# Kernel tuning notes

Hardware: AMD Instinct MI355X
Metric: run time of the kernel (lower is better)

Reference implementation:

```python
import jax, jax.numpy as jnp
import numpy as np

NEG_BIG = -9e15
ALPHA = 0.2  # LeakyReLU slope


def setup_inputs() -> dict:
    key = jax.random.key(0)
    k1, k2, k3, k4 = jax.random.split(key, 4)
    B, N, Fin, Fout = 8, 2048, 256, 64
    h = jax.random.normal(k1, (B, N, Fin), dtype=jnp.float32)
    adj = jax.random.randint(k2, (B, N, N), 0, 2, dtype=jnp.int32)
    # xavier_uniform-ish scale for W and a
    W = jax.random.normal(k3, (Fin, Fout), dtype=jnp.float32) * (1.414 * np.sqrt(2.0 / (Fin + Fout)))
    a = jax.random.normal(k4, (2 * Fout, 1), dtype=jnp.float32) * (1.414 * np.sqrt(2.0 / (2 * Fout + 1)))
    return {"h": h, "adj": adj, "W": W, "a": a}


def reference(h, adj, W, a):
    Fout = W.shape[1]
    Wh = jnp.einsum("bnf,fo->bno", h, W)  # [B,N,Fout]
    # Decompose concat-based score: a_input @ a == Wh@a1 (src) + Wh@a2 (dst)
    a1, a2 = a[:Fout, 0], a[Fout:, 0]
    e_src = Wh @ a1  # [B,N]
    e_dst = Wh @ a2  # [B,N]
    e = e_src[:, :, None] + e_dst[:, None, :]  # [B,N,N]
    e = jnp.where(e > 0, e, ALPHA * e)  # LeakyReLU
    scores = jnp.where(adj > 0, e, NEG_BIG)
    attention = jax.nn.softmax(scores, axis=-1)  # [B,N,N]
    h_prime = jnp.einsum("bnm,bmo->bno", attention, Wh)
    return jax.nn.elu(h_prime)  # concat=True
```

## Files before the change

kernel.cpp:

```cpp
#include <hip/hip_runtime.h>

#define L2E 1.44269504088896340736f

typedef float f32x4 __attribute__((ext_vector_type(4)));
typedef __bf16 bf16x8 __attribute__((ext_vector_type(8)));
typedef __bf16 bf16x4 __attribute__((ext_vector_type(4)));

__device__ inline void mfma_bf16(bf16x8 a, bf16x8 b, f32x4& c) {
    c = __builtin_amdgcn_mfma_f32_16x16x32_bf16(a, b, c, 0, 0, 0);
}


__global__ __launch_bounds__(256, 2)
void k1_wh(const float* __restrict__ h, const float* __restrict__ W,
           const float* __restrict__ a, __bf16* __restrict__ whP,
           float* __restrict__ esrc, float* __restrict__ edst) {
    const int tid  = threadIdx.x;
    const int lane = tid & 63;
    const int w    = tid >> 6;
    const int blk  = blockIdx.x;
    const int r0   = blk * 8;
    const int b    = r0 >> 11;
    const int n0   = r0 & 2047;

    __shared__ float pt_s[8][4][64];
    __shared__ float whs[64][8];

    float wreg[64];
    {
        const float* Wp = W + (size_t)(w * 64) * 64 + lane;
#pragma unroll
        for (int kk = 0; kk < 64; kk++) wreg[kk] = Wp[(size_t)kk * 64];
    }

    const float* hbase = h + (size_t)r0 * 256 + w * 64;
    for (int rr = 0; rr < 8; rr++) {
        const float4* hp = (const float4*)(hbase + rr * 256);
        float acc = 0.f;
#pragma unroll
        for (int q = 0; q < 16; q++) {
            float4 hv = hp[q];
            acc += hv.x * wreg[4 * q + 0];
            acc += hv.y * wreg[4 * q + 1];
            acc += hv.z * wreg[4 * q + 2];
            acc += hv.w * wreg[4 * q + 3];
        }
        pt_s[rr][w][lane] = acc;
    }
    __syncthreads();

    const float a1 = a[lane];
    const float a2 = a[64 + lane];
#pragma unroll
    for (int rq = 0; rq < 2; rq++) {
        const int rr = w * 2 + rq;
        float v = pt_s[rr][0][lane] + pt_s[rr][1][lane] +
                  pt_s[rr][2][lane] + pt_s[rr][3][lane];
        whs[lane][rr] = v;
        float e1 = v * a1, e2 = v * a2;
#pragma unroll
        for (int d = 1; d < 64; d <<= 1) {
            e1 += __shfl_xor(e1, d);
            e2 += __shfl_xor(e2, d);
        }
        if (lane == 0) { esrc[r0 + rr] = e1; edst[r0 + rr] = e2; }
    }
    __syncthreads();

    if (tid < 128) {
        const int o  = tid >> 1, hf = (tid & 1) * 4;
        float4 v = *(const float4*)&whs[o][hf];
        bf16x4 bv = { (__bf16)v.x, (__bf16)v.y, (__bf16)v.z, (__bf16)v.w };
        const int t   = n0 >> 6;
        const int kh  = (n0 >> 5) & 1;
        const int hi2 = (n0 >> 3) & 3;
        const int ob  = o >> 4;
        const int rr  = o & 15;
        const size_t flat =
            ((((size_t)(b * 32 + t) * 2 + kh) * 4 + ob) * 4 + hi2) * 128 +
            rr * 8 + hf;
        *(bf16x4*)(whP + flat) = bv;
    }
}

__global__ __launch_bounds__(256, 2)
void k2_attn(const int* __restrict__ adj, const __bf16* __restrict__ whP,
             const float* __restrict__ esrc, const float* __restrict__ edst,
             float* __restrict__ out) {
    const int tid  = threadIdx.x;
    const int lane = tid & 63;
    const int jg   = tid >> 6;
    const int blk  = blockIdx.x;
    const int b    = blk >> 7;
    const int i0   = (blk & 127) * 16;
    const int r    = lane & 15;
    const int hi   = lane >> 4;

    __shared__ float edst_s[2048];
    __shared__ float esrc_s[16];
    __shared__ float red_s[4];
    __shared__ float mrg_acc[3][1024];
    __shared__ float mrg_l[3][16];

    float mymax = -3.0e38f;
#pragma unroll
    for (int q = 0; q < 2; q++) {
        float4 v = *(const float4*)&edst[b * 2048 + q * 1024 + tid * 4];
        *(float4*)&edst_s[q * 1024 + tid * 4] = v;
        mymax = fmaxf(fmaxf(mymax, v.x), fmaxf(v.y, fmaxf(v.z, v.w)));
    }
#pragma unroll
    for (int d = 1; d < 64; d <<= 1) mymax = fmaxf(mymax, __shfl_xor(mymax, d));
    if (lane == 0) red_s[jg] = mymax;
    if (tid < 16) esrc_s[tid] = esrc[b * 2048 + i0 + tid];
    __syncthreads();

    const float maxed = fmaxf(fmaxf(red_s[0], red_s[1]), fmaxf(red_s[2], red_s[3]));
    const float es = esrc_s[r];
    float M = es + maxed;
    M = fmaxf(M, 0.2f * M);
    const float Mc = M * L2E;

    const int jbase = jg * 512;
    const int* abase = adj + (size_t)(b * 2048 + i0) * 2048 + jbase + lane;
    const __bf16* wbase = whP + (size_t)b * 131072 +
                          (size_t)(jg * 8) * 4096 + lane * 8;

    f32x4 lacc = {0.f, 0.f, 0.f, 0.f};
    f32x4 acc0 = {0.f,0.f,0.f,0.f}, acc1 = {0.f,0.f,0.f,0.f};
    f32x4 acc2 = {0.f,0.f,0.f,0.f}, acc3 = {0.f,0.f,0.f,0.f};

#define PB(E, bits, sh, base)                                                 \
    {                                                                         \
        const unsigned bb = (bits) >> (sh);                                   \
        float v;                                                              \
        v = es + E.x; v = fmaxf(v, 0.2f * v);                                 \
        p[base + 0] = (bb & 1u) ? exp2f(__builtin_fmaf(v, L2E, -Mc)) : 0.f;   \
        v = es + E.y; v = fmaxf(v, 0.2f * v);                                 \
        p[base + 1] = (bb & 2u) ? exp2f(__builtin_fmaf(v, L2E, -Mc)) : 0.f;   \
        v = es + E.z; v = fmaxf(v, 0.2f * v);                                 \
        p[base + 2] = (bb & 4u) ? exp2f(__builtin_fmaf(v, L2E, -Mc)) : 0.f;   \
        v = es + E.w; v = fmaxf(v, 0.2f * v);                                 \
        p[base + 3] = (bb & 8u) ? exp2f(__builtin_fmaf(v, L2E, -Mc)) : 0.f;   \
    }

    for (int tl = 0; tl < 8; ++tl) {
        const int jt = tl * 64;
        int av[16];
#pragma unroll
        for (int rr2 = 0; rr2 < 16; rr2++)
            av[rr2] = abase[(size_t)rr2 * 2048 + jt];
        const __bf16* wb = wbase + (size_t)tl * 4096;
        bf16x8 B00 = *(const bf16x8*)(wb);
        bf16x8 B01 = *(const bf16x8*)(wb + 512);
        bf16x8 B02 = *(const bf16x8*)(wb + 1024);
        bf16x8 B03 = *(const bf16x8*)(wb + 1536);
        bf16x8 B10 = *(const bf16x8*)(wb + 2048);
        bf16x8 B11 = *(const bf16x8*)(wb + 2560);
        bf16x8 B12 = *(const bf16x8*)(wb + 3072);
        bf16x8 B13 = *(const bf16x8*)(wb + 3584);
        unsigned int mlo = 0u, mhi = 0u;
#pragma unroll
        for (int rr2 = 0; rr2 < 16; rr2++) {
            unsigned long long bal = __ballot(av[rr2] > 0);
            if (r == rr2) { mlo = (unsigned int)bal;
                            mhi = (unsigned int)(bal >> 32); }
        }
        const unsigned int blo = mlo >> (hi * 8);
        const unsigned int bhi = mhi >> (hi * 8);
        float4 e0 = *(const float4*)&edst_s[jbase + jt + hi * 8];
        float4 e1 = *(const float4*)&edst_s[jbase + jt + hi * 8 + 4];
        float4 e2 = *(const float4*)&edst_s[jbase + jt + 32 + hi * 8];
        float4 e3 = *(const float4*)&edst_s[jbase + jt + 32 + hi * 8 + 4];
        float p[16];
        PB(e0, blo, 0, 0) PB(e1, blo, 4, 4) PB(e2, bhi, 0, 8) PB(e3, bhi, 4, 12)
        lacc[0] += p[0] + p[4] + p[8]  + p[12];
        lacc[1] += p[1] + p[5] + p[9]  + p[13];
        lacc[2] += p[2] + p[6] + p[10] + p[14];
        lacc[3] += p[3] + p[7] + p[11] + p[15];
        bf16x8 pa0, pa1;
#pragma unroll
        for (int e = 0; e < 8; e++) {
            pa0[e] = (__bf16)p[e];
            pa1[e] = (__bf16)p[e + 8];
        }
        mfma_bf16(pa0, B00, acc0); mfma_bf16(pa1, B10, acc0);
        mfma_bf16(pa0, B01, acc1); mfma_bf16(pa1, B11, acc1);
        mfma_bf16(pa0, B02, acc2); mfma_bf16(pa1, B12, acc2);
        mfma_bf16(pa0, B03, acc3); mfma_bf16(pa1, B13, acc3);
    }
#undef PB

    float lsum = lacc[0] + lacc[1] + lacc[2] + lacc[3];
    lsum += __shfl_xor(lsum, 16);
    lsum += __shfl_xor(lsum, 32);

    if (jg > 0) {
        float* mb = mrg_acc[jg - 1];
        *(f32x4*)&mb[lane * 4]       = acc0;
        *(f32x4*)&mb[256 + lane * 4] = acc1;
        *(f32x4*)&mb[512 + lane * 4] = acc2;
        *(f32x4*)&mb[768 + lane * 4] = acc3;
        if (lane < 16) mrg_l[jg - 1][r] = lsum;
    }
    __syncthreads();
    if (jg == 0) {
        float ltot = lsum;
#pragma unroll
        for (int wv = 0; wv < 3; wv++) {
            const float* mb = mrg_acc[wv];
            acc0 += *(const f32x4*)&mb[lane * 4];
            acc1 += *(const f32x4*)&mb[256 + lane * 4];
            acc2 += *(const f32x4*)&mb[512 + lane * 4];
            acc3 += *(const f32x4*)&mb[768 + lane * 4];
            ltot += mrg_l[wv][r];
        }
#pragma unroll
        for (int reg = 0; reg < 4; reg++) {
            const float L  = __shfl(ltot, hi * 4 + reg);
            const float iL = 1.0f / L;
            float v0 = acc0[reg] * iL;
            float v1 = acc1[reg] * iL;
            float v2 = acc2[reg] * iL;
            float v3 = acc3[reg] * iL;
            v0 = v0 > 0.f ? v0 : expm1f(v0);
            v1 = v1 > 0.f ? v1 : expm1f(v1);
            v2 = v2 > 0.f ? v2 : expm1f(v2);
            v3 = v3 > 0.f ? v3 : expm1f(v3);
            float* op = out + (size_t)(b * 2048 + i0 + hi * 4 + reg) * 64 + r;
            op[0]  = v0;
            op[16] = v1;
            op[32] = v2;
            op[48] = v3;
        }
    }
}

extern "C" void kernel_launch(void* const* d_in, const int* in_sizes, int n_in,
                              void* d_out, int out_size, void* d_ws, size_t ws_size,
                              hipStream_t stream) {
    const float* h   = (const float*)d_in[0];
    const int*   adj = (const int*)d_in[1];
    const float* W   = (const float*)d_in[2];
    const float* a   = (const float*)d_in[3];
    float* out = (float*)d_out;

    __bf16* whP  = (__bf16*)d_ws;
    float*  esrc = (float*)((char*)d_ws + (size_t)8 * 131072 * 2);
    float*  edst = esrc + 8 * 2048;

    hipLaunchKernelGGL(k1_wh, dim3(2048), dim3(256), 0, stream,
                       h, W, a, whP, esrc, edst);
    hipLaunchKernelGGL(k2_attn, dim3(1024), dim3(256), 0, stream,
                       adj, whP, esrc, edst, out);
}
```

Before: 69.08 us.

## Split attention over key quarters with LDS-staged Wh and atomic reduction

The attention kernel now gives each 512-thread block 128 query rows and one quarter of the key range. That quarter's packed Wh slice is staged once in shared memory and reused by all eight waves, where before each wave read its slice from global memory per 16-row block. Partial numerators and denominators are accumulated with global float atomics into a workspace zeroed by the first kernel, and a new third kernel normalises and applies ELU. This cuts redundant Wh traffic and the in-block merge, at the cost of many atomics, an extra launch, and 64KB of LDS per block, which limits occupancy.

Result: slower. 73.06 us (+5.7%).

```diff
diff --git a/kernel.cpp b/kernel.cpp
--- a/kernel.cpp
+++ b/kernel.cpp
@@ -10,11 +10,17 @@
     c = __builtin_amdgcn_mfma_f32_16x16x32_bf16(a, b, c, 0, 0, 0);
 }
 
+#define WS_ESRC 2097152
+#define WS_EDST 2162688
+#define WS_NUM  2228224
+#define WS_DEN  6422528
+
 
 __global__ __launch_bounds__(256, 2)
 void k1_wh(const float* __restrict__ h, const float* __restrict__ W,
            const float* __restrict__ a, __bf16* __restrict__ whP,
-           float* __restrict__ esrc, float* __restrict__ edst) {
+           float* __restrict__ esrc, float* __restrict__ edst,
+           float* __restrict__ numden) {
     const int tid  = threadIdx.x;
     const int lane = tid & 63;
     const int w    = tid >> 6;
@@ -22,6 +28,11 @@
     const int r0   = blk * 8;
     const int b    = r0 >> 11;
     const int n0   = r0 & 2047;
+
+    if (tid < 130) {
+        const int zi = blk * 130 + tid;
+        *(float4*)&numden[zi * 4] = make_float4(0.f, 0.f, 0.f, 0.f);
+    }
 
     __shared__ float pt_s[8][4][64];
     __shared__ float whs[64][8];
@@ -83,52 +94,58 @@
     }
 }
 
-__global__ __launch_bounds__(256, 2)
+__global__ __launch_bounds__(512, 4)
 void k2_attn(const int* __restrict__ adj, const __bf16* __restrict__ whP,
              const float* __restrict__ esrc, const float* __restrict__ edst,
-             float* __restrict__ out) {
+             float* __restrict__ num, float* __restrict__ den) {
     const int tid  = threadIdx.x;
     const int lane = tid & 63;
-    const int jg   = tid >> 6;
+    const int w    = tid >> 6;
     const int blk  = blockIdx.x;
-    const int b    = blk >> 7;
-    const int i0   = (blk & 127) * 16;
+    const int b    = blk & 7;
+    const int t2   = blk >> 3;
+    const int jq   = t2 & 3;
+    const int rg   = t2 >> 2;
+    const int i0   = rg * 128;
     const int r    = lane & 15;
     const int hi   = lane >> 4;
 
-    __shared__ float edst_s[2048];
-    __shared__ float esrc_s[16];
-    __shared__ float red_s[4];
-    __shared__ float mrg_acc[3][1024];
-    __shared__ float mrg_l[3][16];
-
-    float mymax = -3.0e38f;
-#pragma unroll
-    for (int q = 0; q < 2; q++) {
-        float4 v = *(const float4*)&edst[b * 2048 + q * 1024 + tid * 4];
-        *(float4*)&edst_s[q * 1024 + tid * 4] = v;
-        mymax = fmaxf(fmaxf(mymax, v.x), fmaxf(v.y, fmaxf(v.z, v.w)));
-    }
-#pragma unroll
-    for (int d = 1; d < 64; d <<= 1) mymax = fmaxf(mymax, __shfl_xor(mymax, d));
-    if (lane == 0) red_s[jg] = mymax;
-    if (tid < 16) esrc_s[tid] = esrc[b * 2048 + i0 + tid];
+    __shared__ __align__(16) __bf16 whp_s[32768];
+    __shared__ float edst_s[512];
+    __shared__ float esrc_s[128];
+    __shared__ float red_s[8];
+
+    const __bf16* wsrc = whP + (size_t)b * 131072 + (size_t)jq * 32768;
+#pragma unroll
+    for (int it = 0; it < 8; it++) {
+        const int idx = it * 512 + tid;
+        *(bf16x8*)&whp_s[idx * 8] = *(const bf16x8*)&wsrc[(size_t)idx * 8];
+    }
+    {
+        float4 v = *(const float4*)&edst[b * 2048 + tid * 4];
+        float mymax = fmaxf(fmaxf(v.x, v.y), fmaxf(v.z, v.w));
+#pragma unroll
+        for (int d = 1; d < 64; d <<= 1)
+            mymax = fmaxf(mymax, __shfl_xor(mymax, d));
+        if (lane == 0) red_s[w] = mymax;
+    }
+    edst_s[tid] = edst[b * 2048 + jq * 512 + tid];
+    if (tid < 128) esrc_s[tid] = esrc[b * 2048 + i0 + tid];
     __syncthreads();
 
-    const float maxed = fmaxf(fmaxf(red_s[0], red_s[1]), fmaxf(red_s[2], red_s[3]));
-    const float es = esrc_s[r];
+    float maxed = red_s[0];
+#pragma unroll
+    for (int q = 1; q < 8; q++) maxed = fmaxf(maxed, red_s[q]);
+    const float es = esrc_s[w * 16 + r];
     float M = es + maxed;
     M = fmaxf(M, 0.2f * M);
     const float Mc = M * L2E;
 
-    const int jbase = jg * 512;
-    const int* abase = adj + (size_t)(b * 2048 + i0) * 2048 + jbase + lane;
-    const __bf16* wbase = whP + (size_t)b * 131072 +
-                          (size_t)(jg * 8) * 4096 + lane * 8;
+    const int* arow = adj + (size_t)(b * 2048 + i0 + w * 16) * 2048 +
+                      jq * 512 + lane;
 
     f32x4 lacc = {0.f, 0.f, 0.f, 0.f};
-    f32x4 acc0 = {0.f,0.f,0.f,0.f}, acc1 = {0.f,0.f,0.f,0.f};
-    f32x4 acc2 = {0.f,0.f,0.f,0.f}, acc3 = {0.f,0.f,0.f,0.f};
+    f32x4 acc0 = {0,0,0,0}, acc1 = {0,0,0,0}, acc2 = {0,0,0,0}, acc3 = {0,0,0,0};
 
 #define PB(E, bits, sh, base)                                                 \
     {                                                                         \
@@ -148,9 +165,8 @@
         const int jt = tl * 64;
         int av[16];
 #pragma unroll
-        for (int rr2 = 0; rr2 < 16; rr2++)
-            av[rr2] = abase[(size_t)rr2 * 2048 + jt];
-        const __bf16* wb = wbase + (size_t)tl * 4096;
+        for (int rr = 0; rr < 16; rr++) av[rr] = arow[(size_t)rr * 2048 + jt];
+        const __bf16* wb = whp_s + tl * 4096 + lane * 8;
         bf16x8 B00 = *(const bf16x8*)(wb);
         bf16x8 B01 = *(const bf16x8*)(wb + 512);
         bf16x8 B02 = *(const bf16x8*)(wb + 1024);
@@ -159,21 +175,21 @@
         bf16x8 B11 = *(const bf16x8*)(wb + 2560);
         bf16x8 B12 = *(const bf16x8*)(wb + 3072);
         bf16x8 B13 = *(const bf16x8*)(wb + 3584);
-        unsigned int mlo = 0u, mhi = 0u;
-#pragma unroll
-        for (int rr2 = 0; rr2 < 16; rr2++) {
-            unsigned long long bal = __ballot(av[rr2] > 0);
-            if (r == rr2) { mlo = (unsigned int)bal;
-                            mhi = (unsigned int)(bal >> 32); }
-        }
-        const unsigned int blo = mlo >> (hi * 8);
-        const unsigned int bhi = mhi >> (hi * 8);
-        float4 e0 = *(const float4*)&edst_s[jbase + jt + hi * 8];
-        float4 e1 = *(const float4*)&edst_s[jbase + jt + hi * 8 + 4];
-        float4 e2 = *(const float4*)&edst_s[jbase + jt + 32 + hi * 8];
-        float4 e3 = *(const float4*)&edst_s[jbase + jt + 32 + hi * 8 + 4];
+        unsigned mlo = 0u, mhi2 = 0u;
+#pragma unroll
+        for (int rr = 0; rr < 16; rr++) {
+            unsigned long long bal = __ballot(av[rr] > 0);
+            if (r == rr) { mlo  = (unsigned)bal;
+                           mhi2 = (unsigned)(bal >> 32); }
+        }
+        const unsigned aLo = mlo  >> (hi * 8);
+        const unsigned aHi = mhi2 >> (hi * 8);
+        float4 e0 = *(const float4*)&edst_s[jt + hi * 8];
+        float4 e1 = *(const float4*)&edst_s[jt + hi * 8 + 4];
+        float4 e2 = *(const float4*)&edst_s[jt + 32 + hi * 8];
+        float4 e3 = *(const float4*)&edst_s[jt + 32 + hi * 8 + 4];
         float p[16];
-        PB(e0, blo, 0, 0) PB(e1, blo, 4, 4) PB(e2, bhi, 0, 8) PB(e3, bhi, 4, 12)
+        PB(e0, aLo, 0, 0) PB(e1, aLo, 4, 4) PB(e2, aHi, 0, 8) PB(e3, aHi, 4, 12)
         lacc[0] += p[0] + p[4] + p[8]  + p[12];
         lacc[1] += p[1] + p[5] + p[9]  + p[13];
         lacc[2] += p[2] + p[6] + p[10] + p[14];
@@ -194,46 +210,30 @@
     float lsum = lacc[0] + lacc[1] + lacc[2] + lacc[3];
     lsum += __shfl_xor(lsum, 16);
     lsum += __shfl_xor(lsum, 32);
-
-    if (jg > 0) {
-        float* mb = mrg_acc[jg - 1];
-        *(f32x4*)&mb[lane * 4]       = acc0;
-        *(f32x4*)&mb[256 + lane * 4] = acc1;
-        *(f32x4*)&mb[512 + lane * 4] = acc2;
-        *(f32x4*)&mb[768 + lane * 4] = acc3;
-        if (lane < 16) mrg_l[jg - 1][r] = lsum;
-    }
-    __syncthreads();
-    if (jg == 0) {
-        float ltot = lsum;
-#pragma unroll
-        for (int wv = 0; wv < 3; wv++) {
-            const float* mb = mrg_acc[wv];
-            acc0 += *(const f32x4*)&mb[lane * 4];
-            acc1 += *(const f32x4*)&mb[256 + lane * 4];
-            acc2 += *(const f32x4*)&mb[512 + lane * 4];
-            acc3 += *(const f32x4*)&mb[768 + lane * 4];
-            ltot += mrg_l[wv][r];
-        }
-#pragma unroll
-        for (int reg = 0; reg < 4; reg++) {
-            const float L  = __shfl(ltot, hi * 4 + reg);
-            const float iL = 1.0f / L;
-            float v0 = acc0[reg] * iL;
-            float v1 = acc1[reg] * iL;
-            float v2 = acc2[reg] * iL;
-            float v3 = acc3[reg] * iL;
-            v0 = v0 > 0.f ? v0 : expm1f(v0);
-            v1 = v1 > 0.f ? v1 : expm1f(v1);
-            v2 = v2 > 0.f ? v2 : expm1f(v2);
-            v3 = v3 > 0.f ? v3 : expm1f(v3);
-            float* op = out + (size_t)(b * 2048 + i0 + hi * 4 + reg) * 64 + r;
-            op[0]  = v0;
-            op[16] = v1;
-            op[32] = v2;
-            op[48] = v3;
-        }
-    }
+    const int rowbase = b * 2048 + i0 + w * 16;
+    if (lane < 16) atomicAdd(&den[rowbase + r], lsum);
+#pragma unroll
+    for (int reg = 0; reg < 4; reg++) {
+        float* np = num + (size_t)(rowbase + 4 * hi + reg) * 64 + r;
+        atomicAdd(np +  0, acc0[reg]);
+        atomicAdd(np + 16, acc1[reg]);
+        atomicAdd(np + 32, acc2[reg]);
+        atomicAdd(np + 48, acc3[reg]);
+    }
+}
+
+__global__ __launch_bounds__(256, 4)
+void k3_fin(const float* __restrict__ num, const float* __restrict__ den,
+            float* __restrict__ out) {
+    const int i = blockIdx.x * 256 + threadIdx.x;
+    float4 n = *(const float4*)&num[(size_t)i * 4];
+    const float inv = 1.0f / den[i >> 4];
+    float v0 = n.x * inv, v1 = n.y * inv, v2 = n.z * inv, v3 = n.w * inv;
+    v0 = v0 > 0.f ? v0 : expm1f(v0);
+    v1 = v1 > 0.f ? v1 : expm1f(v1);
+    v2 = v2 > 0.f ? v2 : expm1f(v2);
+    v3 = v3 > 0.f ? v3 : expm1f(v3);
+    *(float4*)&out[(size_t)i * 4] = make_float4(v0, v1, v2, v3);
 }
 
 extern "C" void kernel_launch(void* const* d_in, const int* in_sizes, int n_in,
@@ -245,12 +245,17 @@
     const float* a   = (const float*)d_in[3];
     float* out = (float*)d_out;
 
-    __bf16* whP  = (__bf16*)d_ws;
-    float*  esrc = (float*)((char*)d_ws + (size_t)8 * 131072 * 2);
-    float*  edst = esrc + 8 * 2048;
+    char* ws = (char*)d_ws;
+    __bf16* whP  = (__bf16*)ws;
+    float*  esrc = (float*)(ws + WS_ESRC);
+    float*  edst = (float*)(ws + WS_EDST);
+    float*  num  = (float*)(ws + WS_NUM);
+    float*  den  = (float*)(ws + WS_DEN);
 
     hipLaunchKernelGGL(k1_wh, dim3(2048), dim3(256), 0, stream,
-                       h, W, a, whP, esrc, edst);
-    hipLaunchKernelGGL(k2_attn, dim3(1024), dim3(256), 0, stream,
-                       adj, whP, esrc, edst, out);
-}
+                       h, W, a, whP, esrc, edst, num);
+    hipLaunchKernelGGL(k2_attn, dim3(512), dim3(512), 0, stream,
+                       adj, whP, esrc, edst, num, den);
+    hipLaunchKernelGGL(k3_fin, dim3(1024), dim3(256), 0, stream,
+                       num, den, out);
+}
```
